# Performance work log

Measured on AMD Instinct MI355X. Metric: run time of the kernel, lower is better.

Reference implementation:

```python
import jax, jax.numpy as jnp
import numpy as np

NUM_GROUPS = 32
NUM_HEADS = 8
EPS = 1e-5


def setup_inputs() -> dict:
    key = jax.random.key(0)
    ks = jax.random.split(key, 4)
    b, c, h, w = 16, 512, 32, 32
    x = jax.random.normal(ks[0], (b, c, h, w), dtype=jnp.float32)
    norm_w = jnp.ones((c,), dtype=jnp.float32)
    norm_b = jnp.zeros((c,), dtype=jnp.float32)
    qkv_w = jax.random.normal(ks[1], (3 * c, c), dtype=jnp.float32) * (1.0 / np.sqrt(c))
    qkv_b = jnp.zeros((3 * c,), dtype=jnp.float32)
    proj_w = jax.random.normal(ks[2], (c, c), dtype=jnp.float32) * (1.0 / np.sqrt(c))
    proj_b = jnp.zeros((c,), dtype=jnp.float32)
    return {"x": x, "norm_w": norm_w, "norm_b": norm_b,
            "qkv_w": qkv_w, "qkv_b": qkv_b, "proj_w": proj_w, "proj_b": proj_b}


def group_norm(x, weight, bias):
    b, c, h, w = x.shape
    xg = x.reshape(b, NUM_GROUPS, c // NUM_GROUPS, h * w)
    mean = xg.mean(axis=(2, 3), keepdims=True)
    var = xg.var(axis=(2, 3), keepdims=True)
    xn = (xg - mean) * jax.lax.rsqrt(var + EPS)
    xn = xn.reshape(b, c, h, w)
    return xn * weight[None, :, None, None] + bias[None, :, None, None]


def reference(x, norm_w, norm_b, qkv_w, qkv_b, proj_w, proj_b):
    b, c, h, w = x.shape
    n = h * w
    head = NUM_HEADS
    ch = c // head

    x_norm = group_norm(x, norm_w, norm_b)
    # 1x1 conv == channel matmul: [b,3c,n]
    xf = x_norm.reshape(b, c, n)
    qkv = jnp.einsum('oc,bcn->bon', qkv_w, xf) + qkv_b[None, :, None]
    q, k, v = jnp.split(qkv, 3, axis=1)  # each [b,c,n]
    q = q.reshape(b, head, ch, n) * (ch ** -0.5)
    k = k.reshape(b, head, ch, n)
    v = v.reshape(b, head, ch, n)

    attn = jnp.einsum('bhcn,bhcm->bhnm', q, k)
    attn = jax.nn.softmax(attn, axis=-1)
    out = jnp.einsum('bhnm,bhcm->bhcn', attn, v)  # [b,head,ch,n]
    out = out.reshape(b, c, n)
    out = jnp.einsum('oc,bcn->bon', proj_w, out) + proj_b[None, :, None]
    return x + out.reshape(b, c, h, w)
```

## Files before the change

kernel.cpp:

```cpp
#include <hip/hip_runtime.h>

typedef short short8 __attribute__((ext_vector_type(8)));
typedef short short4v __attribute__((ext_vector_type(4)));
typedef float f32x4 __attribute__((ext_vector_type(4)));

#define B_   16
#define C_   512
#define N_   1024
#define NH_  8
#define CH_  64
#define G_   32
#define CPG_ 16

__device__ inline float b2f(unsigned int u) {
    union { unsigned int i; float f; } v; v.i = u << 16; return v.f;
}
__device__ inline unsigned short f2b(float f) {
    union { float f; unsigned int i; } v; v.f = f;
    unsigned int r = v.i + 0x7fffu + ((v.i >> 16) & 1u);
    return (unsigned short)(r >> 16);
}
__device__ inline unsigned int pack2(float a, float b) {
    return (unsigned int)f2b(a) | ((unsigned int)f2b(b) << 16);
}
__device__ inline unsigned int asu(float f) {
    union { float f; unsigned int i; } v; v.f = f; return v.i;
}
__device__ inline unsigned int packtr(float a, float b) {
    return __builtin_amdgcn_perm(asu(b), asu(a), 0x07060302u);
}
__device__ inline void gload16(const void* g, void* l) {
    __builtin_amdgcn_global_load_lds(
        (const __attribute__((address_space(1))) void*)g,
        (__attribute__((address_space(3))) void*)l, 16, 0, 0);
}

__global__ __launch_bounds__(256) void gnconv_kernel(const float* __restrict__ x,
                                                     const float* __restrict__ nw,
                                                     const float* __restrict__ nb,
                                                     unsigned short* __restrict__ xnT,
                                                     const float* __restrict__ qkvw,
                                                     const float* __restrict__ projw,
                                                     unsigned short* __restrict__ wq,
                                                     unsigned short* __restrict__ wp)
{
    __shared__ float red[8];
    int t = threadIdx.x;

    if (blockIdx.x >= 512) {
        const int NQ = 3 * C_ * C_;
        int idx = (((int)blockIdx.x - 512) * 256 + t) * 8;
        const float* src; unsigned short* dst; int j;
        if (idx < NQ) { src = qkvw;  dst = wq; j = idx; }
        else          { src = projw; dst = wp; j = idx - NQ; }
        float4 u0 = *(const float4*)(src + j);
        float4 u1 = *(const float4*)(src + j + 4);
        uint4 p;
        p.x = pack2(u0.x, u0.y); p.y = pack2(u0.z, u0.w);
        p.z = pack2(u1.x, u1.y); p.w = pack2(u1.z, u1.w);
        *(uint4*)(dst + j) = p;
        return;
    }

    int b = blockIdx.x >> 5, g = blockIdx.x & 31;
    const float* base = x + ((size_t)(b * C_ + g * CPG_)) * N_;

    float2 v[2][16];
    float s = 0.f, ss = 0.f;
#pragma unroll
    for (int nbi = 0; nbi < 2; ++nbi)
#pragma unroll
        for (int ch = 0; ch < 16; ++ch) {
            float2 u = *(const float2*)(base + (size_t)ch * N_ + nbi * 512 + t * 2);
            v[nbi][ch] = u;
            s  += u.x + u.y;
            ss += u.x * u.x + u.y * u.y;
        }
#pragma unroll
    for (int off = 1; off < 64; off <<= 1) {
        s  += __shfl_xor(s, off);
        ss += __shfl_xor(ss, off);
    }
    int wv = t >> 6;
    if ((t & 63) == 0) { red[wv * 2] = s; red[wv * 2 + 1] = ss; }
    __syncthreads();
    s  = red[0] + red[2] + red[4] + red[6];
    ss = red[1] + red[3] + red[5] + red[7];
    float mean = s * (1.f / 16384.f);
    float var  = ss * (1.f / 16384.f) - mean * mean;
    float rstd = rsqrtf(var + 1e-5f);

    float sc[16], sh[16];
#pragma unroll
    for (int ch = 0; ch < 16; ++ch) {
        sc[ch] = nw[g * CPG_ + ch] * rstd;
        sh[ch] = nb[g * CPG_ + ch] - mean * sc[ch];
    }

#pragma unroll
    for (int nbi = 0; nbi < 2; ++nbi) {
        int n = nbi * 512 + t * 2;
#pragma unroll
        for (int col = 0; col < 2; ++col) {
            float f[16];
#pragma unroll
            for (int ch = 0; ch < 16; ++ch) {
                float xv = col ? v[nbi][ch].y : v[nbi][ch].x;
                f[ch] = xv * sc[ch] + sh[ch];
            }
            uint4 o0, o1;
            o0.x = pack2(f[0], f[1]);  o0.y = pack2(f[2], f[3]);
            o0.z = pack2(f[4], f[5]);  o0.w = pack2(f[6], f[7]);
            o1.x = pack2(f[8], f[9]);  o1.y = pack2(f[10], f[11]);
            o1.z = pack2(f[12], f[13]); o1.w = pack2(f[14], f[15]);
            unsigned short* dst = xnT + ((size_t)(b * N_ + n + col)) * C_ + g * CPG_;
            *(uint4*)dst = o0;
            *(uint4*)(dst + 8) = o1;
        }
    }
}

__global__ __launch_bounds__(256) void qkv_kernel(const unsigned short* __restrict__ w,
                                                  const float* __restrict__ bias,
                                                  const unsigned short* __restrict__ xnT,
                                                  unsigned short* __restrict__ qT,
                                                  unsigned short* __restrict__ kT,
                                                  unsigned short* __restrict__ vv)
{
    __shared__ unsigned short Als[128 * 64], Bls[128 * 64];
    int t = threadIdx.x;
    int n0 = blockIdx.x * 128, m0 = blockIdx.y * 128, b = blockIdx.z;
    int lane = t & 63, wv = t >> 6;
    int l = lane & 15, qd = lane >> 4;
    int wm = (wv >> 1) * 64, wn = (wv & 1) * 64;
    f32x4 acc[4][4] = {};
    const unsigned short* Bbase = xnT + ((size_t)(b * N_ + n0)) * C_;
    int isv = (m0 >= 1024);

    int grow = lane >> 3, gcol = ((lane & 7) ^ grow) * 8;
    const unsigned short* pA[4]; const unsigned short* pB[4];
    unsigned short* lA[4]; unsigned short* lB[4];
#pragma unroll
    for (int g = 0; g < 4; ++g) {
        int r = wv * 32 + g * 8 + grow;
        pA[g] = w + (size_t)(m0 + r) * C_ + gcol;
        pB[g] = Bbase + (size_t)r * C_ + gcol;
        lA[g] = &Als[(wv * 32 + g * 8) * 64];
        lB[g] = &Bls[(wv * 32 + g * 8) * 64];
    }

    for (int kk = 0; kk < 8; ++kk) {
        int ko = kk * 64;
#pragma unroll
        for (int g = 0; g < 4; ++g) {
            gload16(pA[g] + ko, lA[g]);
            gload16(pB[g] + ko, lB[g]);
        }
        __builtin_amdgcn_s_waitcnt(0);
        __syncthreads();
#pragma unroll
        for (int ks = 0; ks < 2; ++ks) {
            short8 aF[4], bF[4];
#pragma unroll
            for (int i = 0; i < 4; ++i) {
                int ra = wm + i * 16 + l;
                aF[i] = *(const short8*)&Als[ra * 64 + (((ks * 4 + qd) ^ (l & 7)) * 8)];
                int rb = wn + i * 16 + l;
                bF[i] = *(const short8*)&Bls[rb * 64 + (((ks * 4 + qd) ^ (l & 7)) * 8)];
            }
            if (!isv) {
#pragma unroll
                for (int mt = 0; mt < 4; ++mt)
#pragma unroll
                    for (int nt = 0; nt < 4; ++nt)
                        acc[mt][nt] = __builtin_amdgcn_mfma_f32_16x16x32_bf16(aF[mt], bF[nt], acc[mt][nt], 0, 0, 0);
            } else {
#pragma unroll
                for (int mt = 0; mt < 4; ++mt)
#pragma unroll
                    for (int nt = 0; nt < 4; ++nt)
                        acc[mt][nt] = __builtin_amdgcn_mfma_f32_16x16x32_bf16(bF[nt], aF[mt], acc[mt][nt], 0, 0, 0);
            }
        }
        __syncthreads();
    }

    if (!isv) {
        int o_base = m0 + wm;
        int sec = o_base >> 9;
        int h = (o_base & 511) >> 6;
        float bv[4][4];
#pragma unroll
        for (int mt = 0; mt < 4; ++mt)
#pragma unroll
            for (int r = 0; r < 4; ++r)
                bv[mt][r] = bias[o_base + mt * 16 + qd * 4 + r];
        unsigned short* dst = (sec == 0) ? qT : kT;
        float scl = (sec == 0) ? (0.125f * 1.44269504f) : 1.0f;
#pragma unroll
        for (int mt = 0; mt < 4; ++mt)
#pragma unroll
            for (int nt = 0; nt < 4; ++nt) {
                int n = n0 + wn + nt * 16 + l;
                ushort4 o;
                o.x = f2b((acc[mt][nt][0] + bv[mt][0]) * scl);
                o.y = f2b((acc[mt][nt][1] + bv[mt][1]) * scl);
                o.z = f2b((acc[mt][nt][2] + bv[mt][2]) * scl);
                o.w = f2b((acc[mt][nt][3] + bv[mt][3]) * scl);
                *(ushort4*)(dst + ((size_t)(b * NH_ + h) * N_ + n) * CH_ + mt * 16 + qd * 4) = o;
            }
    } else {
#pragma unroll
        for (int mt = 0; mt < 4; ++mt) {
            int och = m0 - 1024 + wm + mt * 16;
            int h = och >> 6;
            int chl = (och & 63) + l;
            float bvl = bias[m0 + wm + mt * 16 + l];
            unsigned short* vdst = vv + ((size_t)(b * NH_ + h) * CH_ + chl) * N_;
#pragma unroll
            for (int nt = 0; nt < 4; ++nt) {
                int n = n0 + wn + nt * 16 + qd * 4;
                ushort4 o;
                o.x = f2b(acc[mt][nt][0] + bvl);
                o.y = f2b(acc[mt][nt][1] + bvl);
                o.z = f2b(acc[mt][nt][2] + bvl);
                o.w = f2b(acc[mt][nt][3] + bvl);
                *(ushort4*)(vdst + n) = o;
            }
        }
    }
}

__global__ __launch_bounds__(256, 4) void attn_kernel(const unsigned short* __restrict__ qT,
                                                      const unsigned short* __restrict__ kT,
                                                      const unsigned short* __restrict__ vv,
                                                      unsigned short* __restrict__ at)
{
    __shared__ unsigned short Ks[2][4096];
    __shared__ unsigned short Vs[2][4224];

    int t = threadIdx.x, lane = t & 63, wv = t >> 6;
    int l = lane & 15, qd = lane >> 4;
    int blk = blockIdx.x;
    int ibk = blk >> 7;
    int bh  = blk & 127;
    int h = bh & 7, b = bh >> 3;
    int i0 = ibk * 128 + wv * 32;
    const size_t hoff = (size_t)bh * (size_t)N_ * CH_;
    const unsigned short* qbase = qT + hoff;
    const unsigned short* kbase = kT + hoff;
    const unsigned short* vbase = vv + hoff;

    short8 qF[2][2];
#pragma unroll
    for (int it = 0; it < 2; ++it)
#pragma unroll
        for (int ks = 0; ks < 2; ++ks)
            qF[it][ks] = *(const short8*)(qbase + (size_t)(i0 + it * 16 + l) * CH_ + ks * 32 + qd * 8);

    int srow = t >> 2, p = t & 3;
    int sw = srow & 7, bb = p * 2;
    int d0 = srow * 64 + ((bb ^ sw) * 8);
    int d1 = srow * 64 + (((bb + 1) ^ sw) * 8);
    int lch = srow & 15, chtS = srow >> 4;
    int vblk = p * 4 + chtS;
    int vd[4];
#pragma unroll
    for (int w = 0; w < 4; ++w)
        vd[w] = vblk * 264 + (w * 16 + lch) * 4;
    const unsigned short* kSrc = kbase + (size_t)srow * CH_ + p * 16;
    const unsigned short* vSrc = vbase + (size_t)srow * N_ + p * 16;

    f32x4 Oa[4][2] = {};
    float lsum[2] = {0.f, 0.f};
    int swl = l & 7;

    uint4 ku0, ku1, vu0, vu1;
    {
        const uint4* kp = (const uint4*)(kSrc);
        ku0 = kp[0]; ku1 = kp[1];
        const uint4* vp2 = (const uint4*)(vSrc);
        vu0 = vp2[0]; vu1 = vp2[1];
        *(uint4*)&Ks[0][d0] = ku0; *(uint4*)&Ks[0][d1] = ku1;
        *(uint2*)&Vs[0][vd[0]] = make_uint2(vu0.x, vu0.y);
        *(uint2*)&Vs[0][vd[1]] = make_uint2(vu0.z, vu0.w);
        *(uint2*)&Vs[0][vd[2]] = make_uint2(vu1.x, vu1.y);
        *(uint2*)&Vs[0][vd[3]] = make_uint2(vu1.z, vu1.w);
        kp  = (const uint4*)(kSrc + 4096);
        ku0 = kp[0]; ku1 = kp[1];
        vp2 = (const uint4*)(vSrc + 64);
        vu0 = vp2[0]; vu1 = vp2[1];
    }

    for (int tile = 0; tile < 16; ++tile) {
        __syncthreads();
        if (tile < 15) {
            unsigned short* Kw = Ks[(tile + 1) & 1];
            unsigned short* Vw = Vs[(tile + 1) & 1];
            *(uint4*)&Kw[d0] = ku0; *(uint4*)&Kw[d1] = ku1;
            *(uint2*)&Vw[vd[0]] = make_uint2(vu0.x, vu0.y);
            *(uint2*)&Vw[vd[1]] = make_uint2(vu0.z, vu0.w);
            *(uint2*)&Vw[vd[2]] = make_uint2(vu1.x, vu1.y);
            *(uint2*)&Vw[vd[3]] = make_uint2(vu1.z, vu1.w);
            if (tile < 14) {
                const uint4* kp = (const uint4*)(kSrc + (size_t)(tile + 2) * 4096);
                ku0 = kp[0]; ku1 = kp[1];
                const uint4* vp2 = (const uint4*)(vSrc + (size_t)(tile + 2) * 64);
                vu0 = vp2[0]; vu1 = vp2[1];
            }
        }
        const unsigned short* Kb = Ks[tile & 1];
        const unsigned short* Vb = Vs[tile & 1];
#pragma unroll
        for (int jb = 0; jb < 2; ++jb) {
            short8 kA[2][2];
#pragma unroll
            for (int jt = 0; jt < 2; ++jt)
#pragma unroll
                for (int ks = 0; ks < 2; ++ks)
                    kA[jt][ks] = *(const short8*)&Kb[(jb * 32 + jt * 16 + l) * 64 + (((ks * 4 + qd) ^ swl) * 8)];
            f32x4 Sa[2][2] = {};
#pragma unroll
            for (int jt = 0; jt < 2; ++jt)
#pragma unroll
                for (int it = 0; it < 2; ++it)
#pragma unroll
                    for (int ks = 0; ks < 2; ++ks)
                        Sa[jt][it] = __builtin_amdgcn_mfma_f32_16x16x32_bf16(kA[jt][ks], qF[it][ks], Sa[jt][it], 0, 0, 0);
            unsigned int pk[2][2][2];
#pragma unroll
            for (int jt = 0; jt < 2; ++jt)
#pragma unroll
                for (int it = 0; it < 2; ++it) {
                    float p0 = __builtin_amdgcn_exp2f(Sa[jt][it][0]);
                    float p1 = __builtin_amdgcn_exp2f(Sa[jt][it][1]);
                    float p2 = __builtin_amdgcn_exp2f(Sa[jt][it][2]);
                    float p3 = __builtin_amdgcn_exp2f(Sa[jt][it][3]);
                    lsum[it] += (p0 + p1) + (p2 + p3);
                    pk[jt][it][0] = packtr(p0, p1);
                    pk[jt][it][1] = packtr(p2, p3);
                }
#pragma unroll
            for (int jt = 0; jt < 2; ++jt) {
                short4v vA[4];
#pragma unroll
                for (int cht = 0; cht < 4; ++cht) {
                    union { uint2 u; short4v s; } vr;
                    vr.u = *(const uint2*)&Vb[((jb * 2 + jt) * 4 + cht) * 264 + (qd * 16 + l) * 4];
                    vA[cht] = vr.s;
                }
#pragma unroll
                for (int it = 0; it < 2; ++it) {
                    union { unsigned int u[2]; short4v s; } ap;
                    ap.u[0] = pk[jt][it][0]; ap.u[1] = pk[jt][it][1];
#pragma unroll
                    for (int cht = 0; cht < 4; ++cht)
                        Oa[cht][it] = __builtin_amdgcn_mfma_f32_16x16x16bf16_1k(vA[cht], ap.s, Oa[cht][it], 0, 0, 0);
                }
            }
        }
    }

#pragma unroll
    for (int it = 0; it < 2; ++it) {
        float lt = lsum[it];
        lt += __shfl_xor(lt, 16);
        lt += __shfl_xor(lt, 32);
        float inv = 1.0f / lt;
        int i = i0 + it * 16 + l;
        unsigned short* dst = at + ((size_t)(b * N_ + i)) * C_ + h * CH_;
#pragma unroll
        for (int cht = 0; cht < 4; ++cht) {
            ushort4 o;
            o.x = f2b(Oa[cht][it][0] * inv);
            o.y = f2b(Oa[cht][it][1] * inv);
            o.z = f2b(Oa[cht][it][2] * inv);
            o.w = f2b(Oa[cht][it][3] * inv);
            *(ushort4*)(dst + cht * 16 + qd * 4) = o;
        }
    }
}

__global__ __launch_bounds__(256) void proj_kernel(const unsigned short* __restrict__ w,
                                                   const float* __restrict__ bias,
                                                   const unsigned short* __restrict__ at,
                                                   const float* __restrict__ x,
                                                   float* __restrict__ out)
{
    __shared__ unsigned short Als[128 * 64], Bls[128 * 64];
    int t = threadIdx.x;
    int n0 = blockIdx.x * 128, m0 = blockIdx.y * 128, b = blockIdx.z;
    int lane = t & 63, wv = t >> 6;
    int l = lane & 15, qd = lane >> 4;
    int wm = (wv >> 1) * 64, wn = (wv & 1) * 64;
    f32x4 acc[4][4] = {};
    const unsigned short* Bbase = at + ((size_t)(b * N_ + n0)) * C_;

    int grow = lane >> 3, gcol = ((lane & 7) ^ grow) * 8;
    const unsigned short* pA[4]; const unsigned short* pB[4];
    unsigned short* lA[4]; unsigned short* lB[4];
#pragma unroll
    for (int g = 0; g < 4; ++g) {
        int r = wv * 32 + g * 8 + grow;
        pA[g] = w + (size_t)(m0 + r) * C_ + gcol;
        pB[g] = Bbase + (size_t)r * C_ + gcol;
        lA[g] = &Als[(wv * 32 + g * 8) * 64];
        lB[g] = &Bls[(wv * 32 + g * 8) * 64];
    }

    for (int kk = 0; kk < 8; ++kk) {
        int ko = kk * 64;
#pragma unroll
        for (int g = 0; g < 4; ++g) {
            gload16(pA[g] + ko, lA[g]);
            gload16(pB[g] + ko, lB[g]);
        }
        __builtin_amdgcn_s_waitcnt(0);
        __syncthreads();
#pragma unroll
        for (int ks = 0; ks < 2; ++ks) {
            short8 aF[4], bF[4];
#pragma unroll
            for (int i = 0; i < 4; ++i) {
                int ra = wm + i * 16 + l;
                aF[i] = *(const short8*)&Als[ra * 64 + (((ks * 4 + qd) ^ (l & 7)) * 8)];
                int rb = wn + i * 16 + l;
                bF[i] = *(const short8*)&Bls[rb * 64 + (((ks * 4 + qd) ^ (l & 7)) * 8)];
            }
#pragma unroll
            for (int mt = 0; mt < 4; ++mt)
#pragma unroll
                for (int nt = 0; nt < 4; ++nt)
                    acc[mt][nt] = __builtin_amdgcn_mfma_f32_16x16x32_bf16(aF[mt], bF[nt], acc[mt][nt], 0, 0, 0);
        }
        __syncthreads();
    }

    float bv[4][4];
#pragma unroll
    for (int mt = 0; mt < 4; ++mt)
#pragma unroll
        for (int r = 0; r < 4; ++r)
            bv[mt][r] = bias[m0 + wm + mt * 16 + qd * 4 + r];

#pragma unroll
    for (int mt = 0; mt < 4; ++mt)
#pragma unroll
        for (int nt = 0; nt < 4; ++nt) {
            int n = n0 + wn + nt * 16 + l;
#pragma unroll
            for (int r = 0; r < 4; ++r) {
                int o = m0 + wm + mt * 16 + qd * 4 + r;
                size_t idx = ((size_t)b * C_ + o) * N_ + n;
                out[idx] = acc[mt][nt][r] + bv[mt][r] + x[idx];
            }
        }
}

extern "C" void kernel_launch(void* const* d_in, const int* in_sizes, int n_in,
                              void* d_out, int out_size, void* d_ws, size_t ws_size,
                              hipStream_t stream) {
    const float* x     = (const float*)d_in[0];
    const float* nw    = (const float*)d_in[1];
    const float* nb    = (const float*)d_in[2];
    const float* qkvw  = (const float*)d_in[3];
    const float* qkvb  = (const float*)d_in[4];
    const float* projw = (const float*)d_in[5];
    const float* projb = (const float*)d_in[6];
    float* out = (float*)d_out;
    char* ws = (char*)d_ws;
    const size_t SZ = (size_t)B_ * N_ * C_ * 2;
    unsigned short* xnT = (unsigned short*)(ws);
    unsigned short* qTp = (unsigned short*)(ws + SZ);
    unsigned short* kTp = (unsigned short*)(ws + 2 * SZ);
    unsigned short* vp  = (unsigned short*)(ws + 3 * SZ);
    unsigned short* atp = (unsigned short*)(ws);
    unsigned short* wq  = (unsigned short*)(ws + 4 * SZ);
    unsigned short* wp  = (unsigned short*)(ws + 4 * SZ + (size_t)3 * C_ * C_ * 2);

    hipLaunchKernelGGL(gnconv_kernel, dim3(1024), dim3(256), 0, stream, x, nw, nb, xnT, qkvw, projw, wq, wp);
    hipLaunchKernelGGL(qkv_kernel,    dim3(8, 12, B_), dim3(256), 0, stream, wq, qkvb, xnT, qTp, kTp, vp);
    hipLaunchKernelGGL(attn_kernel,   dim3(1024), dim3(256), 0, stream, qTp, kTp, vp, atp);
    hipLaunchKernelGGL(proj_kernel,   dim3(8, 4, B_), dim3(256), 0, stream, wp, projb, atp, x, out);
}
```

Before: 207.2 us.

## Restructure attention kernel to 8 waves with 16 query rows each, single-buffered LDS

The attention kernel now runs 512 threads per block, with each wave handling 16 query rows instead of 32, so the per-wave accumulator and score registers are halved. K/V LDS staging goes from double to single buffering, which takes two barriers per tile but only one register prefetch of the next tile. The aim is higher occupancy and more waves to hide latency. In exchange, each K/V LDS fragment is reused across fewer query rows, and the extra barrier per tile reduces overlap between loads and compute.

```diff
diff --git a/kernel.cpp b/kernel.cpp
--- a/kernel.cpp
+++ b/kernel.cpp
@@ -231,13 +231,13 @@
     }
 }
 
-__global__ __launch_bounds__(256, 4) void attn_kernel(const unsigned short* __restrict__ qT,
+__global__ __launch_bounds__(512, 8) void attn_kernel(const unsigned short* __restrict__ qT,
                                                       const unsigned short* __restrict__ kT,
                                                       const unsigned short* __restrict__ vv,
                                                       unsigned short* __restrict__ at)
 {
-    __shared__ unsigned short Ks[2][4096];
-    __shared__ unsigned short Vs[2][4224];
+    __shared__ unsigned short Ks[4096];
+    __shared__ unsigned short Vs[4224];
 
     int t = threadIdx.x, lane = t & 63, wv = t >> 6;
     int l = lane & 15, qd = lane >> 4;
@@ -245,72 +245,45 @@
     int ibk = blk >> 7;
     int bh  = blk & 127;
     int h = bh & 7, b = bh >> 3;
-    int i0 = ibk * 128 + wv * 32;
+    int i0 = ibk * 128 + wv * 16;
     const size_t hoff = (size_t)bh * (size_t)N_ * CH_;
     const unsigned short* qbase = qT + hoff;
     const unsigned short* kbase = kT + hoff;
     const unsigned short* vbase = vv + hoff;
 
-    short8 qF[2][2];
-#pragma unroll
-    for (int it = 0; it < 2; ++it)
-#pragma unroll
-        for (int ks = 0; ks < 2; ++ks)
-            qF[it][ks] = *(const short8*)(qbase + (size_t)(i0 + it * 16 + l) * CH_ + ks * 32 + qd * 8);
-
-    int srow = t >> 2, p = t & 3;
-    int sw = srow & 7, bb = p * 2;
-    int d0 = srow * 64 + ((bb ^ sw) * 8);
-    int d1 = srow * 64 + (((bb + 1) ^ sw) * 8);
-    int lch = srow & 15, chtS = srow >> 4;
-    int vblk = p * 4 + chtS;
-    int vd[4];
-#pragma unroll
-    for (int w = 0; w < 4; ++w)
-        vd[w] = vblk * 264 + (w * 16 + lch) * 4;
-    const unsigned short* kSrc = kbase + (size_t)srow * CH_ + p * 16;
-    const unsigned short* vSrc = vbase + (size_t)srow * N_ + p * 16;
-
-    f32x4 Oa[4][2] = {};
-    float lsum[2] = {0.f, 0.f};
+    short8 qF[2];
+#pragma unroll
+    for (int ks = 0; ks < 2; ++ks)
+        qF[ks] = *(const short8*)(qbase + (size_t)(i0 + l) * CH_ + ks * 32 + qd * 8);
+
+    int srow = t >> 3, c8 = t & 7;
+    int kd = srow * 64 + ((c8 ^ (srow & 7)) * 8);
+    const unsigned short* kSrc = kbase + (size_t)srow * CH_ + c8 * 8;
+    const unsigned short* vSrc = vbase + (size_t)srow * N_ + c8 * 8;
+    int q0 = c8 * 2;
+    int vb0 = (q0 >> 2) * 4 + (srow >> 4);
+    int vb1 = ((q0 + 1) >> 2) * 4 + (srow >> 4);
+    int vd0 = vb0 * 264 + (((q0 & 3) * 16 + (srow & 15))) * 4;
+    int vd1 = vb1 * 264 + ((((q0 + 1) & 3) * 16 + (srow & 15))) * 4;
+
+    f32x4 Oa[4] = {};
+    float lsum = 0.f;
     int swl = l & 7;
 
-    uint4 ku0, ku1, vu0, vu1;
-    {
-        const uint4* kp = (const uint4*)(kSrc);
-        ku0 = kp[0]; ku1 = kp[1];
-        const uint4* vp2 = (const uint4*)(vSrc);
-        vu0 = vp2[0]; vu1 = vp2[1];
-        *(uint4*)&Ks[0][d0] = ku0; *(uint4*)&Ks[0][d1] = ku1;
-        *(uint2*)&Vs[0][vd[0]] = make_uint2(vu0.x, vu0.y);
-        *(uint2*)&Vs[0][vd[1]] = make_uint2(vu0.z, vu0.w);
-        *(uint2*)&Vs[0][vd[2]] = make_uint2(vu1.x, vu1.y);
-        *(uint2*)&Vs[0][vd[3]] = make_uint2(vu1.z, vu1.w);
-        kp  = (const uint4*)(kSrc + 4096);
-        ku0 = kp[0]; ku1 = kp[1];
-        vp2 = (const uint4*)(vSrc + 64);
-        vu0 = vp2[0]; vu1 = vp2[1];
-    }
+    uint4 ku = *(const uint4*)(kSrc);
+    uint4 vu = *(const uint4*)(vSrc);
 
     for (int tile = 0; tile < 16; ++tile) {
+        if (tile > 0) __syncthreads();
+        *(uint4*)&Ks[kd] = ku;
+        *(uint2*)&Vs[vd0] = make_uint2(vu.x, vu.y);
+        *(uint2*)&Vs[vd1] = make_uint2(vu.z, vu.w);
+        if (tile < 15) {
+            ku = *(const uint4*)(kSrc + (size_t)(tile + 1) * 4096);
+            vu = *(const uint4*)(vSrc + (size_t)(tile + 1) * 64);
+        }
         __syncthreads();
-        if (tile < 15) {
-            unsigned short* Kw = Ks[(tile + 1) & 1];
-            unsigned short* Vw = Vs[(tile + 1) & 1];
-            *(uint4*)&Kw[d0] = ku0; *(uint4*)&Kw[d1] = ku1;
-            *(uint2*)&Vw[vd[0]] = make_uint2(vu0.x, vu0.y);
-            *(uint2*)&Vw[vd[1]] = make_uint2(vu0.z, vu0.w);
-            *(uint2*)&Vw[vd[2]] = make_uint2(vu1.x, vu1.y);
-            *(uint2*)&Vw[vd[3]] = make_uint2(vu1.z, vu1.w);
-            if (tile < 14) {
-                const uint4* kp = (const uint4*)(kSrc + (size_t)(tile + 2) * 4096);
-                ku0 = kp[0]; ku1 = kp[1];
-                const uint4* vp2 = (const uint4*)(vSrc + (size_t)(tile + 2) * 64);
-                vu0 = vp2[0]; vu1 = vp2[1];
-            }
-        }
-        const unsigned short* Kb = Ks[tile & 1];
-        const unsigned short* Vb = Vs[tile & 1];
+
 #pragma unroll
         for (int jb = 0; jb < 2; ++jb) {
             short8 kA[2][2];
@@ -318,66 +291,56 @@
             for (int jt = 0; jt < 2; ++jt)
 #pragma unroll
                 for (int ks = 0; ks < 2; ++ks)
-                    kA[jt][ks] = *(const short8*)&Kb[(jb * 32 + jt * 16 + l) * 64 + (((ks * 4 + qd) ^ swl) * 8)];
-            f32x4 Sa[2][2] = {};
+                    kA[jt][ks] = *(const short8*)&Ks[(jb * 32 + jt * 16 + l) * 64 + (((ks * 4 + qd) ^ swl) * 8)];
+            f32x4 Sa[2] = {};
 #pragma unroll
             for (int jt = 0; jt < 2; ++jt)
 #pragma unroll
-                for (int it = 0; it < 2; ++it)
-#pragma unroll
-                    for (int ks = 0; ks < 2; ++ks)
-                        Sa[jt][it] = __builtin_amdgcn_mfma_f32_16x16x32_bf16(kA[jt][ks], qF[it][ks], Sa[jt][it], 0, 0, 0);
-            unsigned int pk[2][2][2];
-#pragma unroll
-            for (int jt = 0; jt < 2; ++jt)
-#pragma unroll
-                for (int it = 0; it < 2; ++it) {
-                    float p0 = __builtin_amdgcn_exp2f(Sa[jt][it][0]);
-                    float p1 = __builtin_amdgcn_exp2f(Sa[jt][it][1]);
-                    float p2 = __builtin_amdgcn_exp2f(Sa[jt][it][2]);
-                    float p3 = __builtin_amdgcn_exp2f(Sa[jt][it][3]);
-                    lsum[it] += (p0 + p1) + (p2 + p3);
-                    pk[jt][it][0] = packtr(p0, p1);
-                    pk[jt][it][1] = packtr(p2, p3);
-                }
+                for (int ks = 0; ks < 2; ++ks)
+                    Sa[jt] = __builtin_amdgcn_mfma_f32_16x16x32_bf16(kA[jt][ks], qF[ks], Sa[jt], 0, 0, 0);
+            unsigned int pk[2][2];
+#pragma unroll
+            for (int jt = 0; jt < 2; ++jt) {
+                float p0 = __builtin_amdgcn_exp2f(Sa[jt][0]);
+                float p1 = __builtin_amdgcn_exp2f(Sa[jt][1]);
+                float p2 = __builtin_amdgcn_exp2f(Sa[jt][2]);
+                float p3 = __builtin_amdgcn_exp2f(Sa[jt][3]);
+                lsum += (p0 + p1) + (p2 + p3);
+                pk[jt][0] = packtr(p0, p1);
+                pk[jt][1] = packtr(p2, p3);
+            }
 #pragma unroll
             for (int jt = 0; jt < 2; ++jt) {
                 short4v vA[4];
 #pragma unroll
                 for (int cht = 0; cht < 4; ++cht) {
                     union { uint2 u; short4v s; } vr;
-                    vr.u = *(const uint2*)&Vb[((jb * 2 + jt) * 4 + cht) * 264 + (qd * 16 + l) * 4];
+                    vr.u = *(const uint2*)&Vs[((jb * 2 + jt) * 4 + cht) * 264 + (qd * 16 + l) * 4];
                     vA[cht] = vr.s;
                 }
-#pragma unroll
-                for (int it = 0; it < 2; ++it) {
-                    union { unsigned int u[2]; short4v s; } ap;
-                    ap.u[0] = pk[jt][it][0]; ap.u[1] = pk[jt][it][1];
-#pragma unroll
-                    for (int cht = 0; cht < 4; ++cht)
-                        Oa[cht][it] = __builtin_amdgcn_mfma_f32_16x16x16bf16_1k(vA[cht], ap.s, Oa[cht][it], 0, 0, 0);
-                }
-            }
-        }
-    }
-
-#pragma unroll
-    for (int it = 0; it < 2; ++it) {
-        float lt = lsum[it];
-        lt += __shfl_xor(lt, 16);
-        lt += __shfl_xor(lt, 32);
-        float inv = 1.0f / lt;
-        int i = i0 + it * 16 + l;
-        unsigned short* dst = at + ((size_t)(b * N_ + i)) * C_ + h * CH_;
-#pragma unroll
-        for (int cht = 0; cht < 4; ++cht) {
-            ushort4 o;
-            o.x = f2b(Oa[cht][it][0] * inv);
-            o.y = f2b(Oa[cht][it][1] * inv);
-            o.z = f2b(Oa[cht][it][2] * inv);
-            o.w = f2b(Oa[cht][it][3] * inv);
-            *(ushort4*)(dst + cht * 16 + qd * 4) = o;
-        }
+                union { unsigned int u[2]; short4v s; } ap;
+                ap.u[0] = pk[jt][0]; ap.u[1] = pk[jt][1];
+#pragma unroll
+                for (int cht = 0; cht < 4; ++cht)
+                    Oa[cht] = __builtin_amdgcn_mfma_f32_16x16x16bf16_1k(vA[cht], ap.s, Oa[cht], 0, 0, 0);
+            }
+        }
+    }
+
+    float lt = lsum;
+    lt += __shfl_xor(lt, 16);
+    lt += __shfl_xor(lt, 32);
+    float inv = 1.0f / lt;
+    int i = i0 + l;
+    unsigned short* dst = at + ((size_t)(b * N_ + i)) * C_ + h * CH_;
+#pragma unroll
+    for (int cht = 0; cht < 4; ++cht) {
+        ushort4 o;
+        o.x = f2b(Oa[cht][0] * inv);
+        o.y = f2b(Oa[cht][1] * inv);
+        o.z = f2b(Oa[cht][2] * inv);
+        o.w = f2b(Oa[cht][3] * inv);
+        *(ushort4*)(dst + cht * 16 + qd * 4) = o;
     }
 }
 
@@ -480,6 +443,6 @@
 
     hipLaunchKernelGGL(gnconv_kernel, dim3(1024), dim3(256), 0, stream, x, nw, nb, xnT, qkvw, projw, wq, wp);
     hipLaunchKernelGGL(qkv_kernel,    dim3(8, 12, B_), dim3(256), 0, stream, wq, qkvb, xnT, qTp, kTp, vp);
-    hipLaunchKernelGGL(attn_kernel,   dim3(1024), dim3(256), 0, stream, qTp, kTp, vp, atp);
+    hipLaunchKernelGGL(attn_kernel,   dim3(1024), dim3(512), 0, stream, qTp, kTp, vp, atp);
     hipLaunchKernelGGL(proj_kernel,   dim3(8, 4, B_), dim3(256), 0, stream, wp, projb, atp, x, out);
 }
```

Measured after the change: 220.2 us. +6.3%, slower.
